# Kernel optimization log

Hardware: AMD Instinct MI355X
Metric: run time of the kernel (lower is better)

## Reference

```python
import jax, jax.numpy as jnp
import numpy as np

NEG = -1e30  # finite stand-in for -inf (safe under grads)


def setup_inputs() -> dict:
    key = jax.random.key(0)
    k0, k1, k2, k3 = jax.random.split(key, 4)
    B, L, NS, NG = 32, 1024, 32768, 64
    spans = jax.random.randint(k0, (B, NS, 2), 0, L)
    span_scores = jax.random.normal(k1, (B, NS), dtype=jnp.float32)
    gold_spans = jax.random.randint(k2, (B, NG, 2), 0, L)
    gold_span_labels = jax.random.randint(k3, (B, NG), 0, 2)
    span_mask = jnp.ones((B, NS), jnp.float32)
    gold_span_mask = jnp.ones((B, NG), jnp.float32)
    token_mask = jnp.ones((B, L), jnp.float32)
    return {
        "spans": spans,
        "span_scores": span_scores,
        "gold_spans": gold_spans,
        "gold_span_labels": gold_span_labels,
        "span_mask": span_mask,
        "gold_span_mask": gold_span_mask,
        "token_mask": token_mask,
    }


def _span_table(spans, span_scores, L):
    # T[b, s, e] = sum of span_scores over list entries with (start, end) == (s, e)
    B = span_scores.shape[0]
    b = jnp.arange(B)[:, None]
    T = jnp.zeros((B, L, L), span_scores.dtype)
    return T.at[b, spans[..., 0], spans[..., 1]].add(span_scores)


def _log_denominator(T, token_mask):
    # semi-Markov CRF forward algorithm.
    # beta[i] = logsumexp over last-segment-start j of alpha[i, j]; the original
    # DP only consumes alpha rows through their row-logsumexp, so:
    # beta[i] = logsumexp({beta[s] + S(s, i-1) : s < i} U {beta[i-1] - S(i-1, i-1)})
    B, L = token_mask.shape

    def step(beta, i):
        row = jax.lax.dynamic_index_in_dim(T, i - 1, axis=2, keepdims=False)  # (B, L): S(s, i-1)
        valid = jnp.arange(L) < i
        cand = jnp.where(valid[None, :], beta[:, :L] + row, NEG)
        lse_plus = jax.nn.logsumexp(cand, axis=1)                             # (B,)
        beta_prev = jax.lax.dynamic_index_in_dim(beta, i - 1, axis=1, keepdims=False)
        diag = jax.lax.dynamic_index_in_dim(row, i - 1, axis=1, keepdims=False)  # S(i-1, i-1)
        new_val = jnp.logaddexp(lse_plus, beta_prev - diag)
        beta = jax.lax.dynamic_update_index_in_dim(beta, new_val, i, axis=1)
        return beta, None

    beta0 = jnp.full((B, L + 1), NEG, T.dtype).at[:, 0].set(0.0)
    beta, _ = jax.lax.scan(step, beta0, jnp.arange(1, L + 1))
    n = token_mask.sum(-1).astype(jnp.int32)  # valid length per batch element
    return jnp.take_along_axis(beta, n[:, None], axis=1)[:, 0]


def _log_numerator(T, gold_spans, gold_span_labels, gold_span_mask):
    B = T.shape[0]
    b = jnp.arange(B)[:, None]
    vals = T[b, gold_spans[..., 0], gold_spans[..., 1]]  # (B, NG)
    signs = 2.0 * gold_span_labels.astype(T.dtype) - 1.0
    return jnp.sum(vals * gold_span_mask * signs, axis=1)


def reference(spans, span_scores, gold_spans, gold_span_labels, span_mask, gold_span_mask, token_mask):
    # span_mask is accepted (as in the original forward signature) but unused
    # by the likelihood math in the source.
    L = token_mask.shape[1]
    T = _span_table(spans, span_scores, L)
    log_den = _log_denominator(T, token_mask)
    log_num = _log_numerator(T, gold_spans, gold_span_labels, gold_span_mask)
    return jnp.sum(log_num - log_den)
```

## Files before the change

kernel.cpp:

```cpp
#include <hip/hip_runtime.h>


#define B_   32
#define L_   1024
#define NS_  32768
#define NG_  64
#define CAP_ 128
#define NREC 128

#define DPP_ADD(v, ctrl) \
    ((v) + __int_as_float(__builtin_amdgcn_update_dpp( \
        0, __float_as_int(v), (ctrl), 0xf, 0xf, false)))

__device__ __forceinline__ float wave_sum64(float v) {
    v = DPP_ADD(v, 0x111);
    v = DPP_ADD(v, 0x112);
    v = DPP_ADD(v, 0x114);
    v = DPP_ADD(v, 0x118);
    v = DPP_ADD(v, 0x142);
    v = DPP_ADD(v, 0x143);
    return __int_as_float(__builtin_amdgcn_readlane(__float_as_int(v), 63));
}

__global__ void sbc_scatter(const int2* __restrict__ spans,
                            const float* __restrict__ scores,
                            unsigned int* __restrict__ keys,
                            float* __restrict__ vals) {
    int idx = blockIdx.x * blockDim.x + threadIdx.x;
    int b = idx >> 15;
    int2 se = spans[idx];
    float sc = scores[idx];
    size_t col = ((size_t)b << 10) | (unsigned)se.y;
    unsigned int* kcol = keys + col * CAP_;
    float*        vcol = vals + col * CAP_;
    unsigned int key = (unsigned int)se.x + 1u;
    int h = se.x & (CAP_ - 1);
    for (int p = 0; p < CAP_; ++p) {
        unsigned int old = atomicCAS(&kcol[h], 0u, key);
        if (old == 0u || old == key) { atomicAdd(&vcol[h], sc); break; }
        h = (h + 1) & (CAP_ - 1);
    }
}

__global__ void __launch_bounds__(256) sbc_prep(const unsigned int* __restrict__ keys,
                                                const float* __restrict__ vals,
                                                uint2* __restrict__ rec) {
    const int wv = threadIdx.x >> 6;
    const int lane = threadIdx.x & 63;
    __shared__ uint2 st[4][NREC];
    __shared__ float dnr[4][8];
    const int step = gridDim.x * 4;
    for (int col = blockIdx.x * 4 + wv; col < B_ * L_; col += step) {
        const int e = col & (L_ - 1);
        const unsigned int* kcol = keys + (size_t)col * CAP_;
        const float*        vcol = vals + (size_t)col * CAP_;
        ((uint4*)st[wv])[lane] = make_uint4(0u, 0u, 0u, 0u);
        if (lane < 8) dnr[wv][lane] = 0.f;
        int cnt = 0;
        #pragma unroll
        for (int r = 0; r < 2; ++r) {
            int slot = lane + r * 64;
            unsigned int k = kcol[slot];
            float v = vcol[slot];
            bool occ = (k != 0u);
            int s = (int)k - 1;
            int t = e - s;
            if (occ && t >= 0 && t <= 3) atomicAdd(&dnr[wv][t], v);
            bool far = occ && (t >= 4);
            unsigned long long mb = __ballot(far);
            int pos = cnt + (int)__popcll(mb & ((1ull << lane) - 1ull));
            if (far && pos < NREC - 2)
                st[wv][2 + pos] = make_uint2((unsigned)s, __float_as_uint(expm1f(v)));
            cnt += (int)__popcll(mb);
        }
        if (lane == 0) {
            float d = dnr[wv][0];
            st[wv][0] = make_uint2(__float_as_uint(__expf(d) + __expf(-d) - 1.f),
                                   __float_as_uint(expm1f(dnr[wv][1])));
            st[wv][1] = make_uint2(__float_as_uint(expm1f(dnr[wv][2])),
                                   __float_as_uint(expm1f(dnr[wv][3])));
        }
        ((uint4*)(rec + (size_t)col * NREC))[lane] = ((const uint4*)st[wv])[lane];
    }
}

__global__ void __launch_bounds__(64) sbc_dp(const uint2* __restrict__ rec,
                                             const float* __restrict__ tmask,
                                             float* __restrict__ den) {
    const int b = blockIdx.x;
    const int lane = threadIdx.x;
    __shared__ float xs[L_ + 1];
    const uint4* pb = (const uint4*)rec + (size_t)b * L_ * (NREC / 2);

    if (lane == 0) xs[0] = 1.f;

    float tm = 0.f;
    for (int t = lane; t < L_; t += 64) tm += tmask[b * L_ + t];
    #pragma unroll
    for (int o = 32; o; o >>= 1) tm += __shfl_xor(tm, o, 64);
    int n = (int)(tm + 0.5f);
    n = (n > L_) ? L_ : n;

    uint4 metaS[4];
    #pragma unroll
    for (int c = 0; c < 4; ++c)
        metaS[c] = pb[c * 64 + lane];
    uint4 pkS[8];
    #pragma unroll
    for (int k = 0; k < 8; ++k)
        pkS[(4 + k) & 7] = pb[(4 + k) * 64 + lane];

    float gS[4] = {0.f, 0.f, 0.f, 0.f};
    float Kcur = 0.f;
    float P = 1.f, m = 0.f;
    float xm1 = 1.f, xm2 = 0.f, xm3 = 0.f, xm4 = 0.f;
    const bool gl = (lane >= 1);

    for (int ii = 0; ii < L_; ii += 8) {
        #pragma unroll
        for (int Kc = 0; Kc < 8; ++Kc) {
            const int e = ii + Kc;
            uint4 M = metaS[Kc & 3];
            float Knext = wave_sum64(gS[(Kc + 1) & 3]);
            uint4 pk = pkS[(Kc + 4) & 7];
            int   s0 = gl ? (int)pk.x : 0;
            int   s1 = gl ? (int)pk.z : 0;
            float w0 = gl ? __uint_as_float(pk.y) : 0.f;
            float w1 = gl ? __uint_as_float(pk.w) : 0.f;
            float p = w0 * xs[s0] + w1 * xs[s1];
            metaS[Kc & 3] = pk;
            gS[Kc & 3] = p;
            int cl = e + 12; cl = (cl > L_ - 1) ? (L_ - 1) : cl;
            pkS[(Kc + 4) & 7] = pb[cl * 64 + lane];
            float A = (P + Kcur)
                    + (__uint_as_float(M.y) * xm2 + __uint_as_float(M.z) * xm3)
                    + __uint_as_float(M.w) * xm4;
            float x = fmaf(xm1, __uint_as_float(M.x), A);
            if (lane == 0) xs[e + 1] = x;
            P += x;
            unsigned long long bm = __ballot(x > 0x1p64f);
            if (bm & 1ull) {
                const float s_ = 0x1p-64f;
                x *= s_; xm1 *= s_; xm2 *= s_; xm3 *= s_;
                P *= s_; Knext *= s_;
                gS[0] *= s_; gS[1] *= s_; gS[2] *= s_; gS[3] *= s_;
                m += 44.361419555836498f;
                for (int j = lane; j <= e + 1; j += 64) xs[j] *= s_;
            }
            xm4 = xm3; xm3 = xm2; xm2 = xm1; xm1 = x;
            Kcur = Knext;
        }
    }
    if (lane == 0) den[b] = m + logf(xs[n]);
}

__global__ void __launch_bounds__(1024) sbc_goldfinal(
        const unsigned int* __restrict__ keys,
        const float* __restrict__ vals,
        const int2* __restrict__ gold,
        const int* __restrict__ labels,
        const float* __restrict__ gmask,
        const float* __restrict__ den,
        float* __restrict__ out) {
    const int wv = threadIdx.x >> 6;
    const int lane = threadIdx.x & 63;
    __shared__ float part[16];
    float acc2 = 0.f;
    #pragma unroll
    for (int r = 0; r < 2; ++r) {
        const int b = wv * 2 + r;
        const int gi = b * NG_ + lane;
        int2 se = gold[gi];
        const size_t col = ((size_t)b << 10) | (unsigned)se.y;
        const unsigned int* kcol = keys + col * CAP_;
        const float*        vcol = vals + col * CAP_;
        unsigned int key = (unsigned int)se.x + 1u;
        int h = se.x & (CAP_ - 1);
        float v = 0.f;
        for (int p = 0; p < CAP_; ++p) {
            unsigned int k = kcol[h];
            if (k == key) { v = vcol[h]; break; }
            if (k == 0u) break;
            h = (h + 1) & (CAP_ - 1);
        }
        float acc = v * gmask[gi] * (2.f * (float)labels[gi] - 1.f);
        #pragma unroll
        for (int o = 32; o; o >>= 1) acc += __shfl_xor(acc, o, 64);
        if (lane == 0) acc2 += acc - den[b];
    }
    if (lane == 0) part[wv] = acc2;
    __syncthreads();
    if (threadIdx.x < 64) {
        float v = (lane < 16) ? part[lane] : 0.f;
        #pragma unroll
        for (int o = 8; o; o >>= 1) v += __shfl_xor(v, o, 64);
        if (lane == 0) out[0] = v;
    }
}

extern "C" void kernel_launch(void* const* d_in, const int* in_sizes, int n_in,
                              void* d_out, int out_size, void* d_ws, size_t ws_size,
                              hipStream_t stream) {
    const int2*  spans       = (const int2*)d_in[0];
    const float* span_scores = (const float*)d_in[1];
    const int2*  gold        = (const int2*)d_in[2];
    const int*   glabels     = (const int*)d_in[3];
    const float* gmask       = (const float*)d_in[5];
    const float* tmask       = (const float*)d_in[6];
    float* out = (float*)d_out;
    (void)in_sizes; (void)n_in; (void)out_size; (void)ws_size;

    char* ws = (char*)d_ws;
    const size_t keysB = (size_t)B_ * L_ * CAP_ * 4;
    const size_t valsB = keysB;
    const size_t recB  = (size_t)B_ * L_ * NREC * 8;
    unsigned int* keys = (unsigned int*)(ws);
    float*        vals = (float*)(ws + keysB);
    uint2*        recp = (uint2*)(ws + keysB + valsB);
    float*        den  = (float*)(ws + keysB + valsB + recB);

    hipMemsetAsync(keys, 0, keysB + valsB, stream);
    sbc_scatter<<<(B_ * NS_) / 256, 256, 0, stream>>>(spans, span_scores, keys, vals);
    sbc_prep<<<2048, 256, 0, stream>>>(keys, vals, recp);
    sbc_dp<<<B_, 64, 0, stream>>>(recp, tmask, den);
    sbc_goldfinal<<<1, 1024, 0, stream>>>(keys, vals, gold, glabels, gmask, den, out);
}
```

Measured before the change: 378.3 us.

## Fuse gold-score lookup into scatter, skip upper spans, prefetch DP gathers

The gold-span numerator is now computed inside the scatter kernel. Each block builds a small shared-memory hash of the gold cells and accumulates matching span scores into it, so the separate gold lookup over the global hash is no longer needed. The scatter skips spans with start greater than end, since they never feed the DP, and blocks are interleaved across batches. The DP kernel loads the xs gather values one step ahead so the LDS reads overlap the wave reduction. The cost is extra shared-memory probing for every span, plus atomic adds into per-batch numerator sums.

Measured after the change: 328.5 us. -13.1%, faster.

```diff
diff --git a/kernel.cpp b/kernel.cpp
--- a/kernel.cpp
+++ b/kernel.cpp
@@ -6,7 +6,6 @@
 #define NS_  32768
 #define NG_  64
 #define CAP_ 128
-#define NREC 128
 
 #define DPP_ADD(v, ctrl) \
     ((v) + __int_as_float(__builtin_amdgcn_update_dpp( \
@@ -22,54 +21,104 @@
     return __int_as_float(__builtin_amdgcn_readlane(__float_as_int(v), 63));
 }
 
-__global__ void sbc_scatter(const int2* __restrict__ spans,
-                            const float* __restrict__ scores,
-                            unsigned int* __restrict__ keys,
-                            float* __restrict__ vals) {
-    int idx = blockIdx.x * blockDim.x + threadIdx.x;
-    int b = idx >> 15;
-    int2 se = spans[idx];
-    float sc = scores[idx];
-    size_t col = ((size_t)b << 10) | (unsigned)se.y;
-    unsigned int* kcol = keys + col * CAP_;
-    float*        vcol = vals + col * CAP_;
-    unsigned int key = (unsigned int)se.x + 1u;
-    int h = se.x & (CAP_ - 1);
-    for (int p = 0; p < CAP_; ++p) {
-        unsigned int old = atomicCAS(&kcol[h], 0u, key);
-        if (old == 0u || old == key) { atomicAdd(&vcol[h], sc); break; }
-        h = (h + 1) & (CAP_ - 1);
+__global__ void __launch_bounds__(256) sbc_scatter(
+        const int2* __restrict__ spans, const float* __restrict__ scores,
+        const int2* __restrict__ gold,  const int* __restrict__ labels,
+        const float* __restrict__ gmask,
+        unsigned int* __restrict__ keys, float* __restrict__ vals,
+        float* __restrict__ num) {
+    const int j = blockIdx.x;
+    const int b = j & 31;
+    const int tid = threadIdx.x;
+    __shared__ unsigned int hkey[128];
+    __shared__ float hval[128];
+    __shared__ int slotof[NG_];
+    if (tid < 128) { hkey[tid] = 0u; hval[tid] = 0.f; }
+    __syncthreads();
+    if (tid < NG_) {
+        int2 se = gold[b * NG_ + tid];
+        unsigned cell = ((unsigned)se.x << 10) | (unsigned)se.y;
+        unsigned key = cell + 1u;
+        unsigned h = (cell * 2654435761u) >> 25;
+        int slot = 0;
+        for (int p = 0; p < 128; ++p) {
+            unsigned old = atomicCAS(&hkey[h], 0u, key);
+            if (old == 0u || old == key) { slot = (int)h; break; }
+            h = (h + 1u) & 127u;
+        }
+        slotof[tid] = slot;
+    }
+    __syncthreads();
+    #pragma unroll
+    for (int r = 0; r < 4; ++r) {
+        const int gi = (b << 15) + ((j >> 5) << 10) + (r << 8) + tid;
+        int2 se = spans[gi];
+        float sc = scores[gi];
+        {
+            unsigned cell = ((unsigned)se.x << 10) | (unsigned)se.y;
+            unsigned key = cell + 1u;
+            unsigned h = (cell * 2654435761u) >> 25;
+            for (int p = 0; p < 128; ++p) {
+                unsigned k = hkey[h];
+                if (k == 0u) break;
+                if (k == key) { atomicAdd(&hval[h], sc); break; }
+                h = (h + 1u) & 127u;
+            }
+        }
+        if (se.x <= se.y) {
+            size_t col = ((size_t)b << 10) | (unsigned)se.y;
+            unsigned int* kcol = keys + col * CAP_;
+            float*        vcol = vals + col * CAP_;
+            unsigned key = (unsigned)se.x + 1u;
+            int h = se.x & (CAP_ - 1);
+            for (int p = 0; p < CAP_; ++p) {
+                unsigned old = atomicCAS(&kcol[h], 0u, key);
+                if (old == 0u || old == key) { atomicAdd(&vcol[h], sc); break; }
+                h = (h + 1) & (CAP_ - 1);
+            }
+        }
+    }
+    __syncthreads();
+    if (tid < NG_) {
+        int g = b * NG_ + tid;
+        float acc = hval[slotof[tid]] * gmask[g] * (2.f * (float)labels[g] - 1.f);
+        #pragma unroll
+        for (int o = 32; o; o >>= 1) acc += __shfl_xor(acc, o, 64);
+        if (tid == 0) atomicAdd(&num[b], acc);
     }
 }
 
 __global__ void __launch_bounds__(256) sbc_prep(const unsigned int* __restrict__ keys,
                                                 const float* __restrict__ vals,
                                                 uint2* __restrict__ rec) {
+    const int j = blockIdx.x;
+    const int b = j & 31;
+    const int cb = (j >> 5) * 16;
     const int wv = threadIdx.x >> 6;
     const int lane = threadIdx.x & 63;
-    __shared__ uint2 st[4][NREC];
+    __shared__ uint2 st[4][CAP_];
     __shared__ float dnr[4][8];
-    const int step = gridDim.x * 4;
-    for (int col = blockIdx.x * 4 + wv; col < B_ * L_; col += step) {
-        const int e = col & (L_ - 1);
-        const unsigned int* kcol = keys + (size_t)col * CAP_;
-        const float*        vcol = vals + (size_t)col * CAP_;
+    for (int cc = 0; cc < 4; ++cc) {
+        const int e = cb + wv * 4 + cc;
+        const size_t col = ((size_t)b << 10) | (unsigned)e;
+        const unsigned int* kcol = keys + col * CAP_;
+        const float*        vcol = vals + col * CAP_;
         ((uint4*)st[wv])[lane] = make_uint4(0u, 0u, 0u, 0u);
         if (lane < 8) dnr[wv][lane] = 0.f;
         int cnt = 0;
         #pragma unroll
         for (int r = 0; r < 2; ++r) {
             int slot = lane + r * 64;
-            unsigned int k = kcol[slot];
+            unsigned k = kcol[slot];
             float v = vcol[slot];
             bool occ = (k != 0u);
             int s = (int)k - 1;
             int t = e - s;
-            if (occ && t >= 0 && t <= 3) atomicAdd(&dnr[wv][t], v);
+            if (occ && t <= 3) atomicAdd(&dnr[wv][t], v);
             bool far = occ && (t >= 4);
             unsigned long long mb = __ballot(far);
             int pos = cnt + (int)__popcll(mb & ((1ull << lane) - 1ull));
-            if (far && pos < NREC - 2)
+            if (far && pos < CAP_ - 2)
                 st[wv][2 + pos] = make_uint2((unsigned)s, __float_as_uint(expm1f(v)));
             cnt += (int)__popcll(mb);
         }
@@ -80,7 +129,7 @@
             st[wv][1] = make_uint2(__float_as_uint(expm1f(dnr[wv][2])),
                                    __float_as_uint(expm1f(dnr[wv][3])));
         }
-        ((uint4*)(rec + (size_t)col * NREC))[lane] = ((const uint4*)st[wv])[lane];
+        ((uint4*)(rec + col * CAP_))[lane] = ((const uint4*)st[wv])[lane];
     }
 }
 
@@ -90,8 +139,9 @@
     const int b = blockIdx.x;
     const int lane = threadIdx.x;
     __shared__ float xs[L_ + 1];
-    const uint4* pb = (const uint4*)rec + (size_t)b * L_ * (NREC / 2);
-
+    const uint4* pb = (const uint4*)rec + (size_t)b * L_ * 64;
+
+    for (int t = lane; t <= L_; t += 64) xs[t] = 0.f;
     if (lane == 0) xs[0] = 1.f;
 
     float tm = 0.f;
@@ -103,14 +153,13 @@
 
     uint4 metaS[4];
     #pragma unroll
-    for (int c = 0; c < 4; ++c)
-        metaS[c] = pb[c * 64 + lane];
+    for (int c = 0; c < 4; ++c) metaS[c] = pb[c * 64 + lane];
     uint4 pkS[8];
     #pragma unroll
-    for (int k = 0; k < 8; ++k)
-        pkS[(4 + k) & 7] = pb[(4 + k) * 64 + lane];
-
-    float gS[4] = {0.f, 0.f, 0.f, 0.f};
+    for (int k = 0; k < 8; ++k) pkS[(4 + k) & 7] = pb[(4 + k) * 64 + lane];
+
+    float gX0[4] = {0,0,0,0}, gX1[4] = {0,0,0,0};
+    float gW0[4] = {0,0,0,0}, gW1[4] = {0,0,0,0};
     float Kcur = 0.f;
     float P = 1.f, m = 0.f;
     float xm1 = 1.f, xm2 = 0.f, xm3 = 0.f, xm4 = 0.f;
@@ -120,16 +169,18 @@
         #pragma unroll
         for (int Kc = 0; Kc < 8; ++Kc) {
             const int e = ii + Kc;
+            const int cs = (Kc + 1) & 3;
+            float p = gW0[cs] * gX0[cs] + gW1[cs] * gX1[cs];
+            float Knext = wave_sum64(p);
             uint4 M = metaS[Kc & 3];
-            float Knext = wave_sum64(gS[(Kc + 1) & 3]);
             uint4 pk = pkS[(Kc + 4) & 7];
-            int   s0 = gl ? (int)pk.x : 0;
-            int   s1 = gl ? (int)pk.z : 0;
-            float w0 = gl ? __uint_as_float(pk.y) : 0.f;
-            float w1 = gl ? __uint_as_float(pk.w) : 0.f;
-            float p = w0 * xs[s0] + w1 * xs[s1];
             metaS[Kc & 3] = pk;
-            gS[Kc & 3] = p;
+            int s0 = (int)(pk.x & 1023u);
+            int s1 = (int)(pk.z & 1023u);
+            gX0[Kc & 3] = xs[s0];
+            gX1[Kc & 3] = xs[s1];
+            gW0[Kc & 3] = gl ? __uint_as_float(pk.y) : 0.f;
+            gW1[Kc & 3] = gl ? __uint_as_float(pk.w) : 0.f;
             int cl = e + 12; cl = (cl > L_ - 1) ? (L_ - 1) : cl;
             pkS[(Kc + 4) & 7] = pb[cl * 64 + lane];
             float A = (P + Kcur)
@@ -143,9 +194,10 @@
                 const float s_ = 0x1p-64f;
                 x *= s_; xm1 *= s_; xm2 *= s_; xm3 *= s_;
                 P *= s_; Knext *= s_;
-                gS[0] *= s_; gS[1] *= s_; gS[2] *= s_; gS[3] *= s_;
+                #pragma unroll
+                for (int q = 0; q < 4; ++q) { gX0[q] *= s_; gX1[q] *= s_; }
                 m += 44.361419555836498f;
-                for (int j = lane; j <= e + 1; j += 64) xs[j] *= s_;
+                for (int jj = lane; jj <= e + 1; jj += 64) xs[jj] *= s_;
             }
             xm4 = xm3; xm3 = xm2; xm2 = xm1; xm1 = x;
             Kcur = Knext;
@@ -154,48 +206,14 @@
     if (lane == 0) den[b] = m + logf(xs[n]);
 }
 
-__global__ void __launch_bounds__(1024) sbc_goldfinal(
-        const unsigned int* __restrict__ keys,
-        const float* __restrict__ vals,
-        const int2* __restrict__ gold,
-        const int* __restrict__ labels,
-        const float* __restrict__ gmask,
-        const float* __restrict__ den,
-        float* __restrict__ out) {
-    const int wv = threadIdx.x >> 6;
-    const int lane = threadIdx.x & 63;
-    __shared__ float part[16];
-    float acc2 = 0.f;
-    #pragma unroll
-    for (int r = 0; r < 2; ++r) {
-        const int b = wv * 2 + r;
-        const int gi = b * NG_ + lane;
-        int2 se = gold[gi];
-        const size_t col = ((size_t)b << 10) | (unsigned)se.y;
-        const unsigned int* kcol = keys + col * CAP_;
-        const float*        vcol = vals + col * CAP_;
-        unsigned int key = (unsigned int)se.x + 1u;
-        int h = se.x & (CAP_ - 1);
-        float v = 0.f;
-        for (int p = 0; p < CAP_; ++p) {
-            unsigned int k = kcol[h];
-            if (k == key) { v = vcol[h]; break; }
-            if (k == 0u) break;
-            h = (h + 1) & (CAP_ - 1);
-        }
-        float acc = v * gmask[gi] * (2.f * (float)labels[gi] - 1.f);
-        #pragma unroll
-        for (int o = 32; o; o >>= 1) acc += __shfl_xor(acc, o, 64);
-        if (lane == 0) acc2 += acc - den[b];
-    }
-    if (lane == 0) part[wv] = acc2;
-    __syncthreads();
-    if (threadIdx.x < 64) {
-        float v = (lane < 16) ? part[lane] : 0.f;
-        #pragma unroll
-        for (int o = 8; o; o >>= 1) v += __shfl_xor(v, o, 64);
-        if (lane == 0) out[0] = v;
-    }
+__global__ void sbc_final(const float* __restrict__ num,
+                          const float* __restrict__ den,
+                          float* __restrict__ out) {
+    int lane = threadIdx.x;
+    float v = (lane < B_) ? (num[lane] - den[lane]) : 0.f;
+    #pragma unroll
+    for (int o = 32; o; o >>= 1) v += __shfl_xor(v, o, 64);
+    if (lane == 0) out[0] = v;
 }
 
 extern "C" void kernel_launch(void* const* d_in, const int* in_sizes, int n_in,
@@ -213,15 +231,16 @@
     char* ws = (char*)d_ws;
     const size_t keysB = (size_t)B_ * L_ * CAP_ * 4;
     const size_t valsB = keysB;
-    const size_t recB  = (size_t)B_ * L_ * NREC * 8;
     unsigned int* keys = (unsigned int*)(ws);
     float*        vals = (float*)(ws + keysB);
-    uint2*        recp = (uint2*)(ws + keysB + valsB);
-    float*        den  = (float*)(ws + keysB + valsB + recB);
-
-    hipMemsetAsync(keys, 0, keysB + valsB, stream);
-    sbc_scatter<<<(B_ * NS_) / 256, 256, 0, stream>>>(spans, span_scores, keys, vals);
+    float*        num  = (float*)(ws + keysB + valsB);
+    float*        den  = num + B_;
+    uint2*        recp = (uint2*)(ws + keysB + valsB + 256);
+
+    hipMemsetAsync(keys, 0, keysB + valsB + B_ * 4, stream);
+    sbc_scatter<<<1024, 256, 0, stream>>>(spans, span_scores, gold, glabels,
+                                          gmask, keys, vals, num);
     sbc_prep<<<2048, 256, 0, stream>>>(keys, vals, recp);
     sbc_dp<<<B_, 64, 0, stream>>>(recp, tmask, den);
-    sbc_goldfinal<<<1, 1024, 0, stream>>>(keys, vals, gold, glabels, gmask, den, out);
-}
+    sbc_final<<<1, 64, 0, stream>>>(num, den, out);
+}
```
